# Kernel optimization log

Measured on AMD Instinct MI355X. Metric: run time of the kernel, lower is better.

## Reference

```python
import jax, jax.numpy as jnp
import numpy as np

EPS = 1e-6


def _ring_view(t, start, length, M):
    # contiguous logical view of `length` oldest positions starting at start
    if start + length <= M:
        return t[:, start:start + length]
    first = t[:, start:]
    return jnp.concatenate([first, t[:, :length - first.shape[1]]], axis=1)


def _ring_write(t, start, chunk, M):
    # write chunk at logical position `start`, wrapping around the ring
    C = chunk.shape[1]
    if start + C <= M:
        return t.at[:, start:start + C].set(chunk)
    first = M - start
    t = t.at[:, start:].set(chunk[:, :first])
    return t.at[:, :C - first].set(chunk[:, first:])


def setup_inputs() -> dict:
    key = jax.random.key(0)
    ks = jax.random.split(key, 9)
    B, M, Hh, D, F, C = 4, 1088, 32, 128, 128, 512
    f = lambda k, s: jax.random.normal(k, s, dtype=jnp.float32)
    return {
        "K": f(ks[0], (B, M, Hh, D)),
        "V": f(ks[1], (B, M, Hh, D)),
        "FK": f(ks[2], (B, M, Hh, F)),
        "H": f(ks[3], (B, Hh, F, D)),
        "S": f(ks[4], (B, Hh, F)),
        "k_c": f(ks[5], (B, C, Hh, D)),
        "v_c": f(ks[6], (B, C, Hh, D)),
        "fk_c": f(ks[7], (B, C, Hh, F)),
        "fq": f(ks[8], (B, C, Hh, F)),
        "write_ptr": 100,
        "valid": 1088,
    }


def reference(K, V, FK, H, S, k_c, v_c, fk_c, fq, write_ptr, valid):
    M = K.shape[1]
    C = k_c.shape[1]
    if valid + C <= M:
        # room left in ring buffer: plain write, no eviction
        pos = (write_ptr + valid) % M
        K = _ring_write(K, pos, k_c, M)
        V = _ring_write(V, pos, v_c, M)
        FK = _ring_write(FK, pos, fk_c, M)
    else:
        # evict num_excess oldest tokens into recurrent state H, S
        num_excess = valid + C - M
        old_fk = _ring_view(FK, write_ptr, num_excess, M)  # (B, E, H, F)
        old_v = _ring_view(V, write_ptr, num_excess, M)    # (B, E, H, D)
        H = H + jnp.einsum('behf,behd->bhfd', old_fk, old_v)
        S = S + old_fk.sum(axis=1)
        write_ptr = (write_ptr + num_excess) % M
        pos = (write_ptr + M) % M  # valid == M now
        K = _ring_write(K, pos, k_c, M)
        V = _ring_write(V, pos, v_c, M)
        FK = _ring_write(FK, pos, fk_c, M)
    # linear_attn_forward(fq)
    y_num = jnp.einsum('bchf,bhfd->bchd', fq, H)
    y_den = jnp.einsum('bchf,bhf->bch', fq, S)[..., None]
    return y_num, y_den, K, V, FK, H, S
```

## Files before the change

### kernel.cpp

```cpp
#include <hip/hip_runtime.h>

typedef float f32x4 __attribute__((ext_vector_type(4)));

constexpr int B  = 4;
constexpr int M  = 1088;
constexpr int HH = 32;
constexpr int D  = 128;
constexpr int F  = 128;
constexpr int C  = 512;

constexpr int SZ_YNUM = B * C * HH * D;
constexpr int SZ_YDEN = B * C * HH;
constexpr int SZ_KVM  = B * M * HH * D;
constexpr int SZ_H    = B * HH * F * D;
constexpr int SZ_S    = B * HH * F;

constexpr int OFF_YNUM = 0;
constexpr int OFF_YDEN = OFF_YNUM + SZ_YNUM;
constexpr int OFF_K    = OFF_YDEN + SZ_YDEN;
constexpr int OFF_V    = OFF_K + SZ_KVM;
constexpr int OFF_FK   = OFF_V + SZ_KVM;
constexpr int OFF_H    = OFF_FK + SZ_KVM;
constexpr int OFF_S    = OFF_H + SZ_H;

constexpr int INNER4      = HH * D / 4;
constexpr int ROWS_PER_CB = 4;
constexpr int COPY_BLOCKS = B * M / ROWS_PER_CB;
constexpr int EPARTS      = 4;
constexpr int HS_BLOCKS   = B * HH * 2 * EPARTS;
constexpr int Y_BLOCKS    = B * HH * 8;

__device__ __forceinline__ void ring_params(const int* wp_p, const int* valid_p,
                                            int& wp, int& num_excess, int& pos) {
    wp = *wp_p;
    int valid = *valid_p;
    if (valid + C <= M) {
        num_excess = 0;
        pos = (wp + valid) % M;
    } else {
        num_excess = valid + C - M;
        pos = (wp + num_excess) % M;
    }
}

__device__ __forceinline__ void ring_copy_block(int cb, int tid,
                                                const f32x4* __restrict__ src,
                                                const f32x4* __restrict__ chk,
                                                f32x4* __restrict__ dst,
                                                int pos) {
    int bm0 = cb * ROWS_PER_CB;
#pragma unroll
    for (int r = 0; r < ROWS_PER_CB; ++r) {
        int bm = bm0 + r;
        int m = bm % M;
        int b = bm / M;
        int off = m - pos;
        if (off < 0) off += M;
        const f32x4* s = (off < C) ? &chk[(b * C + off) * INNER4]
                                   : &src[bm * INNER4];
        f32x4* d = &dst[bm * INNER4];
#pragma unroll
        for (int k = 0; k < INNER4 / 256; ++k)
            d[k * 256 + tid] = s[k * 256 + tid];
    }
}

constexpr int ESTEP = 16;

__device__ void hs_partial_body(int bx,
                                const float* __restrict__ FKi,
                                const float* __restrict__ Vi,
                                float* __restrict__ wsH,
                                float* __restrict__ wsS,
                                int wp, int num_excess) {
    const int tid = threadIdx.x;
    const int epart = bx & (EPARTS - 1);
    int rest = bx >> 2;
    const int fhalf = rest & 1;
    const int bh = rest >> 1;
    const int h = bh & (HH - 1);
    const int b = bh >> 5;
    const int fbase = fhalf * 64;

    const int echunk = (num_excess + EPARTS * ESTEP - 1) / (EPARTS * ESTEP) * ESTEP;
    const int e_lo = epart * echunk;
    const int e_hi_raw = e_lo + echunk;
    const int e_hi = (e_hi_raw < num_excess) ? e_hi_raw : num_excess;

    __shared__ float  fk_s[ESTEP][64];
    __shared__ f32x4  v_s[ESTEP][32];
    __shared__ float  sred[4][64];

    const int tf = tid >> 5;
    const int td = tid & 31;
    const int cq = tid & 63;
    const int qq = tid >> 6;

    f32x4 acc[8];
#pragma unroll
    for (int i = 0; i < 8; ++i) acc[i] = (f32x4)0.f;
    float s_part = 0.f;

    float fk_r[4];
    f32x4 v_r[2];

    auto load_tile = [&](int e0) {
#pragma unroll
        for (int j = 0; j < 4; ++j) {
            int e = e0 + qq + 4 * j;
            int me = wp + e;
            if (me >= M) me -= M;
            if (me >= M) me -= M;
            float v = 0.f;
            if (e < e_hi) v = FKi[((b * M + me) * HH + h) * F + fbase + cq];
            fk_r[j] = v;
        }
#pragma unroll
        for (int j = 0; j < 2; ++j) {
            int e = e0 + tf + 8 * j;
            int me = wp + e;
            if (me >= M) me -= M;
            if (me >= M) me -= M;
            f32x4 v = (f32x4)0.f;
            if (e < e_hi) v = *(const f32x4*)&Vi[((b * M + me) * HH + h) * D + td * 4];
            v_r[j] = v;
        }
    };
    auto store_tile = [&]() {
#pragma unroll
        for (int j = 0; j < 4; ++j) fk_s[qq + 4 * j][cq] = fk_r[j];
#pragma unroll
        for (int j = 0; j < 2; ++j) v_s[tf + 8 * j][td] = v_r[j];
    };

    if (e_lo < e_hi) {
        load_tile(e_lo);
        store_tile();
        for (int e0 = e_lo; e0 < e_hi; e0 += ESTEP) {
            bool more = (e0 + ESTEP < e_hi);
            if (more) load_tile(e0 + ESTEP);
            __syncthreads();
#pragma unroll
            for (int ee = 0; ee < ESTEP; ++ee) {
                f32x4 fa = *(const f32x4*)&fk_s[ee][tf * 8];
                f32x4 fb = *(const f32x4*)&fk_s[ee][tf * 8 + 4];
                f32x4 vv = v_s[ee][td];
                acc[0] += fa.x * vv; acc[1] += fa.y * vv;
                acc[2] += fa.z * vv; acc[3] += fa.w * vv;
                acc[4] += fb.x * vv; acc[5] += fb.y * vv;
                acc[6] += fb.z * vv; acc[7] += fb.w * vv;
            }
#pragma unroll
            for (int j = 0; j < 4; ++j) s_part += fk_s[qq * 4 + j][cq];
            __syncthreads();
            if (more) store_tile();
        }
    }

    sred[qq][cq] = s_part;
    __syncthreads();
    if (tid < 64) {
        wsS[epart * SZ_S + (b * HH + h) * F + fbase + tid] =
            sred[0][tid] + sred[1][tid] + sred[2][tid] + sred[3][tid];
    }

    float* wsHp = wsH + epart * SZ_H;
#pragma unroll
    for (int i = 0; i < 8; ++i) {
        int f = fbase + tf * 8 + i;
        int base = ((b * HH + h) * F + f) * D + td * 4;
        *(f32x4*)&wsHp[base] = acc[i];
    }
}

__device__ void compute_y_den_body(int bx,
                                   const float* __restrict__ fq,
                                   const float* __restrict__ Hi,
                                   const float* __restrict__ Si,
                                   const float* __restrict__ wsH,
                                   const float* __restrict__ wsS,
                                   float* __restrict__ Ho,
                                   float* __restrict__ So,
                                   float* __restrict__ ynum,
                                   float* __restrict__ yden) {
    const int tid = threadIdx.x;
    int t0 = bx;
    const int ct = t0 & 7; t0 >>= 3;
    const int h = t0 & (HH - 1);
    const int b = t0 >> 5;
    const int c0 = ct * 64;
    const int bh = b * HH + h;

    __shared__ float  fq_s[32][65];
    __shared__ f32x4  h_s[32][32];
    __shared__ float  S_s[128];
    __shared__ float  den_s[64][4];

    const int tc = tid >> 5;
    const int td = tid & 31;
    const int cq = tid & 63;
    const int qq = tid >> 6;

    if (tid < 128) {
        float s = Si[bh * F + tid]
                + wsS[0 * SZ_S + bh * F + tid] + wsS[1 * SZ_S + bh * F + tid]
                + wsS[2 * SZ_S + bh * F + tid] + wsS[3 * SZ_S + bh * F + tid];
        S_s[tid] = s;
        if (ct == 0) So[bh * F + tid] = s;
    }

    f32x4 acc[8];
#pragma unroll
    for (int i = 0; i < 8; ++i) acc[i] = (f32x4)0.f;
    float den_part = 0.f;

    for (int f0 = 0; f0 < F; f0 += 32) {
#pragma unroll
        for (int r = 0; r < 8; ++r) {
            int idx = tid + r * 256;
            int cc = idx >> 5, ee = idx & 31;
            fq_s[ee][cc] = fq[((b * C + c0 + cc) * HH + h) * F + f0 + ee];
        }
#pragma unroll
        for (int r = 0; r < 4; ++r) {
            int idx = tid + r * 256;
            int row = idx >> 5, col = idx & 31;
            int base = ((bh) * F + f0 + row) * D + col * 4;
            f32x4 v = *(const f32x4*)&Hi[base];
            v += *(const f32x4*)&wsH[0 * SZ_H + base];
            v += *(const f32x4*)&wsH[1 * SZ_H + base];
            v += *(const f32x4*)&wsH[2 * SZ_H + base];
            v += *(const f32x4*)&wsH[3 * SZ_H + base];
            h_s[row][col] = v;
            if (ct == 0) *(f32x4*)&Ho[base] = v;
        }
        __syncthreads();
#pragma unroll
        for (int ee = 0; ee < 32; ++ee) {
            f32x4 hv = h_s[ee][td];
#pragma unroll
            for (int i = 0; i < 8; ++i) {
                float q = fq_s[ee][tc * 8 + i];
                acc[i] += q * hv;
            }
        }
#pragma unroll
        for (int j = 0; j < 8; ++j)
            den_part += fq_s[qq * 8 + j][cq] * S_s[f0 + qq * 8 + j];
        __syncthreads();
    }

    den_s[cq][qq] = den_part;
    __syncthreads();
    if (tid < 64)
        yden[(b * C + c0 + tid) * HH + h] =
            den_s[tid][0] + den_s[tid][1] + den_s[tid][2] + den_s[tid][3];

#pragma unroll
    for (int i = 0; i < 8; ++i) {
        int c = c0 + tc * 8 + i;
        int base = ((b * C + c) * HH + h) * D + td * 4;
        *(f32x4*)&ynum[base] = acc[i];
    }
}

__global__ __launch_bounds__(256) void fused_hs_vfk(
        const float* __restrict__ FKi, const float* __restrict__ Vi,
        float* __restrict__ wsH,       float* __restrict__ wsS,
        const f32x4* __restrict__ V4,  const f32x4* __restrict__ vc,  f32x4* __restrict__ oV,
        const f32x4* __restrict__ FK4, const f32x4* __restrict__ fkc, f32x4* __restrict__ oFK,
        const int* __restrict__ wp_p,  const int* __restrict__ valid_p) {
    int wp, num_excess, pos;
    ring_params(wp_p, valid_p, wp, num_excess, pos);

    int bx = blockIdx.x;
    if (bx < HS_BLOCKS) {
        hs_partial_body(bx, FKi, Vi, wsH, wsS, wp, num_excess);
        return;
    }
    bx -= HS_BLOCKS;
    if (bx < COPY_BLOCKS) {
        ring_copy_block(bx, threadIdx.x, V4, vc, oV, pos);
        return;
    }
    bx -= COPY_BLOCKS;
    ring_copy_block(bx, threadIdx.x, FK4, fkc, oFK, pos);
}

__global__ __launch_bounds__(256) void fused_y_k(
        const float* __restrict__ fq, const float* __restrict__ Hi,
        const float* __restrict__ Si,
        const float* __restrict__ wsH, const float* __restrict__ wsS,
        float* __restrict__ Ho,        float* __restrict__ So,
        float* __restrict__ ynum,      float* __restrict__ yden,
        const f32x4* __restrict__ K4,  const f32x4* __restrict__ kc,
        f32x4* __restrict__ oK,
        const int* __restrict__ wp_p,  const int* __restrict__ valid_p) {
    int wp, num_excess, pos;
    ring_params(wp_p, valid_p, wp, num_excess, pos);

    int bx = blockIdx.x;
    if (bx < Y_BLOCKS) {
        compute_y_den_body(bx, fq, Hi, Si, wsH, wsS, Ho, So, ynum, yden);
        return;
    }
    bx -= Y_BLOCKS;
    ring_copy_block(bx, threadIdx.x, K4, kc, oK, pos);
}

extern "C" void kernel_launch(void* const* d_in, const int* in_sizes, int n_in,
                              void* d_out, int out_size, void* d_ws, size_t ws_size,
                              hipStream_t stream) {
    const float* K   = (const float*)d_in[0];
    const float* V   = (const float*)d_in[1];
    const float* FK  = (const float*)d_in[2];
    const float* H   = (const float*)d_in[3];
    const float* S   = (const float*)d_in[4];
    const float* k_c = (const float*)d_in[5];
    const float* v_c = (const float*)d_in[6];
    const float* fk_c= (const float*)d_in[7];
    const float* fq  = (const float*)d_in[8];
    const int* wp    = (const int*)d_in[9];
    const int* valid = (const int*)d_in[10];

    float* out = (float*)d_out;
    float* o_ynum = out + OFF_YNUM;
    float* o_yden = out + OFF_YDEN;
    float* o_K    = out + OFF_K;
    float* o_V    = out + OFF_V;
    float* o_FK   = out + OFF_FK;
    float* o_H    = out + OFF_H;
    float* o_S    = out + OFF_S;

    float* wsH = (float*)d_ws;
    float* wsS = wsH + EPARTS * SZ_H;

    fused_hs_vfk<<<HS_BLOCKS + 2 * COPY_BLOCKS, 256, 0, stream>>>(
        FK, V, wsH, wsS,
        (const f32x4*)V,  (const f32x4*)v_c,  (f32x4*)o_V,
        (const f32x4*)FK, (const f32x4*)fk_c, (f32x4*)o_FK,
        wp, valid);

    fused_y_k<<<Y_BLOCKS + COPY_BLOCKS, 256, 0, stream>>>(
        fq, H, S, wsH, wsS, o_H, o_S, o_ynum, o_yden,
        (const f32x4*)K, (const f32x4*)k_c, (f32x4*)o_K,
        wp, valid);
}
```

Before: 157.5 us.

## Split H/S reduction into its own pass and double-buffer the H accumulation tiles

```diff
diff --git a/kernel.cpp b/kernel.cpp
--- a/kernel.cpp
+++ b/kernel.cpp
@@ -29,6 +29,7 @@
 constexpr int EPARTS      = 4;
 constexpr int HS_BLOCKS   = B * HH * 2 * EPARTS;
 constexpr int Y_BLOCKS    = B * HH * 8;
+constexpr int RED_BLOCKS  = 256;
 
 __device__ __forceinline__ void ring_params(const int* wp_p, const int* valid_p,
                                             int& wp, int& num_excess, int& pos) {
@@ -87,8 +88,8 @@
     const int e_hi_raw = e_lo + echunk;
     const int e_hi = (e_hi_raw < num_excess) ? e_hi_raw : num_excess;
 
-    __shared__ float  fk_s[ESTEP][64];
-    __shared__ f32x4  v_s[ESTEP][32];
+    __shared__ float  fk_s[2][ESTEP][64];
+    __shared__ f32x4  v_s[2][ESTEP][32];
     __shared__ float  sred[4][64];
 
     const int tf = tid >> 5;
@@ -101,10 +102,10 @@
     for (int i = 0; i < 8; ++i) acc[i] = (f32x4)0.f;
     float s_part = 0.f;
 
-    float fk_r[4];
-    f32x4 v_r[2];
-
-    auto load_tile = [&](int e0) {
+    float fkA[4], fkB[4];
+    f32x4 vA[2],  vB[2];
+
+    auto load_tile = [&](int e0, float* fk_r, f32x4* v_r) {
 #pragma unroll
         for (int j = 0; j < 4; ++j) {
             int e = e0 + qq + 4 * j;
@@ -126,34 +127,42 @@
             v_r[j] = v;
         }
     };
-    auto store_tile = [&]() {
-#pragma unroll
-        for (int j = 0; j < 4; ++j) fk_s[qq + 4 * j][cq] = fk_r[j];
-#pragma unroll
-        for (int j = 0; j < 2; ++j) v_s[tf + 8 * j][td] = v_r[j];
+    auto store_tile = [&](const float* fk_r, const f32x4* v_r, int buf) {
+#pragma unroll
+        for (int j = 0; j < 4; ++j) fk_s[buf][qq + 4 * j][cq] = fk_r[j];
+#pragma unroll
+        for (int j = 0; j < 2; ++j) v_s[buf][tf + 8 * j][td] = v_r[j];
     };
+    auto compute = [&](int buf) {
+#pragma unroll
+        for (int ee = 0; ee < ESTEP; ++ee) {
+            f32x4 fa = *(const f32x4*)&fk_s[buf][ee][tf * 8];
+            f32x4 fb = *(const f32x4*)&fk_s[buf][ee][tf * 8 + 4];
+            f32x4 vv = v_s[buf][ee][td];
+            acc[0] += fa.x * vv; acc[1] += fa.y * vv;
+            acc[2] += fa.z * vv; acc[3] += fa.w * vv;
+            acc[4] += fb.x * vv; acc[5] += fb.y * vv;
+            acc[6] += fb.z * vv; acc[7] += fb.w * vv;
+        }
+#pragma unroll
+        for (int j = 0; j < 4; ++j) s_part += fk_s[buf][qq * 4 + j][cq];
+    };
 
     if (e_lo < e_hi) {
-        load_tile(e_lo);
-        store_tile();
-        for (int e0 = e_lo; e0 < e_hi; e0 += ESTEP) {
-            bool more = (e0 + ESTEP < e_hi);
-            if (more) load_tile(e0 + ESTEP);
+        const int nt = (e_hi - e_lo + ESTEP - 1) / ESTEP;
+        load_tile(e_lo, fkA, vA);
+        if (nt > 1) load_tile(e_lo + ESTEP, fkB, vB);
+        store_tile(fkA, vA, 0);
+        for (int t = 0; t < nt; t += 2) {
             __syncthreads();
-#pragma unroll
-            for (int ee = 0; ee < ESTEP; ++ee) {
-                f32x4 fa = *(const f32x4*)&fk_s[ee][tf * 8];
-                f32x4 fb = *(const f32x4*)&fk_s[ee][tf * 8 + 4];
-                f32x4 vv = v_s[ee][td];
-                acc[0] += fa.x * vv; acc[1] += fa.y * vv;
-                acc[2] += fa.z * vv; acc[3] += fa.w * vv;
-                acc[4] += fb.x * vv; acc[5] += fb.y * vv;
-                acc[6] += fb.z * vv; acc[7] += fb.w * vv;
-            }
-#pragma unroll
-            for (int j = 0; j < 4; ++j) s_part += fk_s[qq * 4 + j][cq];
+            if (t + 1 < nt) store_tile(fkB, vB, 1);
+            if (t + 2 < nt) load_tile(e_lo + (t + 2) * ESTEP, fkA, vA);
+            compute(0);
+            if (t + 1 >= nt) break;
             __syncthreads();
-            if (more) store_tile();
+            if (t + 2 < nt) store_tile(fkA, vA, 0);
+            if (t + 3 < nt) load_tile(e_lo + (t + 3) * ESTEP, fkB, vB);
+            compute(1);
         }
     }
 
@@ -175,12 +184,8 @@
 
 __device__ void compute_y_den_body(int bx,
                                    const float* __restrict__ fq,
-                                   const float* __restrict__ Hi,
-                                   const float* __restrict__ Si,
-                                   const float* __restrict__ wsH,
-                                   const float* __restrict__ wsS,
-                                   float* __restrict__ Ho,
-                                   float* __restrict__ So,
+                                   const float* __restrict__ Hn,
+                                   const float* __restrict__ Sn,
                                    float* __restrict__ ynum,
                                    float* __restrict__ yden) {
     const int tid = threadIdx.x;
@@ -201,13 +206,7 @@
     const int cq = tid & 63;
     const int qq = tid >> 6;
 
-    if (tid < 128) {
-        float s = Si[bh * F + tid]
-                + wsS[0 * SZ_S + bh * F + tid] + wsS[1 * SZ_S + bh * F + tid]
-                + wsS[2 * SZ_S + bh * F + tid] + wsS[3 * SZ_S + bh * F + tid];
-        S_s[tid] = s;
-        if (ct == 0) So[bh * F + tid] = s;
-    }
+    if (tid < 128) S_s[tid] = Sn[bh * F + tid];
 
     f32x4 acc[8];
 #pragma unroll
@@ -225,14 +224,7 @@
         for (int r = 0; r < 4; ++r) {
             int idx = tid + r * 256;
             int row = idx >> 5, col = idx & 31;
-            int base = ((bh) * F + f0 + row) * D + col * 4;
-            f32x4 v = *(const f32x4*)&Hi[base];
-            v += *(const f32x4*)&wsH[0 * SZ_H + base];
-            v += *(const f32x4*)&wsH[1 * SZ_H + base];
-            v += *(const f32x4*)&wsH[2 * SZ_H + base];
-            v += *(const f32x4*)&wsH[3 * SZ_H + base];
-            h_s[row][col] = v;
-            if (ct == 0) *(f32x4*)&Ho[base] = v;
+            h_s[row][col] = *(const f32x4*)&Hn[(bh * F + f0 + row) * D + col * 4];
         }
         __syncthreads();
 #pragma unroll
@@ -287,12 +279,10 @@
     ring_copy_block(bx, threadIdx.x, FK4, fkc, oFK, pos);
 }
 
-__global__ __launch_bounds__(256) void fused_y_k(
-        const float* __restrict__ fq, const float* __restrict__ Hi,
-        const float* __restrict__ Si,
+__global__ __launch_bounds__(256) void fused_red_k(
+        const float* __restrict__ Hi,  const float* __restrict__ Si,
         const float* __restrict__ wsH, const float* __restrict__ wsS,
         float* __restrict__ Ho,        float* __restrict__ So,
-        float* __restrict__ ynum,      float* __restrict__ yden,
         const f32x4* __restrict__ K4,  const f32x4* __restrict__ kc,
         f32x4* __restrict__ oK,
         const int* __restrict__ wp_p,  const int* __restrict__ valid_p) {
@@ -300,12 +290,39 @@
     ring_params(wp_p, valid_p, wp, num_excess, pos);
 
     int bx = blockIdx.x;
-    if (bx < Y_BLOCKS) {
-        compute_y_den_body(bx, fq, Hi, Si, wsH, wsS, Ho, So, ynum, yden);
+    const int tid = threadIdx.x;
+    if (bx < RED_BLOCKS) {
+        constexpr int H4 = SZ_H / 4;
+        const f32x4* h4 = (const f32x4*)Hi;
+        const f32x4* w4 = (const f32x4*)wsH;
+        f32x4* o4 = (f32x4*)Ho;
+        int base = bx * (H4 / RED_BLOCKS) + tid;
+#pragma unroll
+        for (int r = 0; r < H4 / RED_BLOCKS / 256; ++r) {
+            int i = base + r * 256;
+            f32x4 v = h4[i];
+            v += w4[0 * H4 + i];
+            v += w4[1 * H4 + i];
+            v += w4[2 * H4 + i];
+            v += w4[3 * H4 + i];
+            o4[i] = v;
+        }
+        if (bx < SZ_S / 256) {
+            int si = bx * 256 + tid;
+            So[si] = Si[si] + wsS[si] + wsS[SZ_S + si]
+                   + wsS[2 * SZ_S + si] + wsS[3 * SZ_S + si];
+        }
         return;
     }
-    bx -= Y_BLOCKS;
-    ring_copy_block(bx, threadIdx.x, K4, kc, oK, pos);
+    bx -= RED_BLOCKS;
+    ring_copy_block(bx, tid, K4, kc, oK, pos);
+}
+
+__global__ __launch_bounds__(256) void y_kernel(
+        const float* __restrict__ fq, const float* __restrict__ Hn,
+        const float* __restrict__ Sn,
+        float* __restrict__ ynum,     float* __restrict__ yden) {
+    compute_y_den_body(blockIdx.x, fq, Hn, Sn, ynum, yden);
 }
 
 extern "C" void kernel_launch(void* const* d_in, const int* in_sizes, int n_in,
@@ -341,8 +358,10 @@
         (const f32x4*)FK, (const f32x4*)fk_c, (f32x4*)o_FK,
         wp, valid);
 
-    fused_y_k<<<Y_BLOCKS + COPY_BLOCKS, 256, 0, stream>>>(
-        fq, H, S, wsH, wsS, o_H, o_S, o_ynum, o_yden,
+    fused_red_k<<<RED_BLOCKS + COPY_BLOCKS, 256, 0, stream>>>(
+        H, S, wsH, wsS, o_H, o_S,
         (const f32x4*)K, (const f32x4*)k_c, (f32x4*)o_K,
         wp, valid);
-}
+
+    y_kernel<<<Y_BLOCKS, 256, 0, stream>>>(fq, o_H, o_S, o_ynum, o_yden);
+}
```

Measured after the change: 163.6 us, median of 4. +3.9%, slower.

## Reduce H/S partials in a separate kernel and halve eviction partitions

Applied to the files above, without the earlier changes.

```diff
diff --git a/kernel.cpp b/kernel.cpp
--- a/kernel.cpp
+++ b/kernel.cpp
@@ -26,9 +26,10 @@
 constexpr int INNER4      = HH * D / 4;
 constexpr int ROWS_PER_CB = 4;
 constexpr int COPY_BLOCKS = B * M / ROWS_PER_CB;
-constexpr int EPARTS      = 4;
+constexpr int EPARTS      = 2;
 constexpr int HS_BLOCKS   = B * HH * 2 * EPARTS;
 constexpr int Y_BLOCKS    = B * HH * 8;
+constexpr int RED_BLOCKS  = 256;
 
 __device__ __forceinline__ void ring_params(const int* wp_p, const int* valid_p,
                                             int& wp, int& num_excess, int& pos) {
@@ -75,7 +76,7 @@
                                 int wp, int num_excess) {
     const int tid = threadIdx.x;
     const int epart = bx & (EPARTS - 1);
-    int rest = bx >> 2;
+    int rest = bx >> 1;
     const int fhalf = rest & 1;
     const int bh = rest >> 1;
     const int h = bh & (HH - 1);
@@ -175,12 +176,8 @@
 
 __device__ void compute_y_den_body(int bx,
                                    const float* __restrict__ fq,
-                                   const float* __restrict__ Hi,
-                                   const float* __restrict__ Si,
-                                   const float* __restrict__ wsH,
-                                   const float* __restrict__ wsS,
-                                   float* __restrict__ Ho,
-                                   float* __restrict__ So,
+                                   const float* __restrict__ Hn,
+                                   const float* __restrict__ Sn,
                                    float* __restrict__ ynum,
                                    float* __restrict__ yden) {
     const int tid = threadIdx.x;
@@ -201,13 +198,7 @@
     const int cq = tid & 63;
     const int qq = tid >> 6;
 
-    if (tid < 128) {
-        float s = Si[bh * F + tid]
-                + wsS[0 * SZ_S + bh * F + tid] + wsS[1 * SZ_S + bh * F + tid]
-                + wsS[2 * SZ_S + bh * F + tid] + wsS[3 * SZ_S + bh * F + tid];
-        S_s[tid] = s;
-        if (ct == 0) So[bh * F + tid] = s;
-    }
+    if (tid < 128) S_s[tid] = Sn[bh * F + tid];
 
     f32x4 acc[8];
 #pragma unroll
@@ -225,14 +216,7 @@
         for (int r = 0; r < 4; ++r) {
             int idx = tid + r * 256;
             int row = idx >> 5, col = idx & 31;
-            int base = ((bh) * F + f0 + row) * D + col * 4;
-            f32x4 v = *(const f32x4*)&Hi[base];
-            v += *(const f32x4*)&wsH[0 * SZ_H + base];
-            v += *(const f32x4*)&wsH[1 * SZ_H + base];
-            v += *(const f32x4*)&wsH[2 * SZ_H + base];
-            v += *(const f32x4*)&wsH[3 * SZ_H + base];
-            h_s[row][col] = v;
-            if (ct == 0) *(f32x4*)&Ho[base] = v;
+            h_s[row][col] = *(const f32x4*)&Hn[(bh * F + f0 + row) * D + col * 4];
         }
         __syncthreads();
 #pragma unroll
@@ -287,21 +271,42 @@
     ring_copy_block(bx, threadIdx.x, FK4, fkc, oFK, pos);
 }
 
+__global__ __launch_bounds__(256) void red_kernel(
+        const float* __restrict__ Hi,  const float* __restrict__ Si,
+        const float* __restrict__ wsH, const float* __restrict__ wsS,
+        float* __restrict__ Ho,        float* __restrict__ So) {
+    const int bx = blockIdx.x;
+    const int tid = threadIdx.x;
+    constexpr int H4 = SZ_H / 4;
+    const f32x4* h4 = (const f32x4*)Hi;
+    const f32x4* w4 = (const f32x4*)wsH;
+    f32x4* o4 = (f32x4*)Ho;
+    int base = bx * (H4 / RED_BLOCKS) + tid;
+#pragma unroll
+    for (int r = 0; r < H4 / RED_BLOCKS / 256; ++r) {
+        int i = base + r * 256;
+        f32x4 v = h4[i] + w4[i] + w4[H4 + i];
+        o4[i] = v;
+    }
+    if (bx < SZ_S / 256) {
+        int si = bx * 256 + tid;
+        So[si] = Si[si] + wsS[si] + wsS[SZ_S + si];
+    }
+}
+
 __global__ __launch_bounds__(256) void fused_y_k(
-        const float* __restrict__ fq, const float* __restrict__ Hi,
-        const float* __restrict__ Si,
-        const float* __restrict__ wsH, const float* __restrict__ wsS,
-        float* __restrict__ Ho,        float* __restrict__ So,
-        float* __restrict__ ynum,      float* __restrict__ yden,
-        const f32x4* __restrict__ K4,  const f32x4* __restrict__ kc,
+        const float* __restrict__ fq, const float* __restrict__ Hn,
+        const float* __restrict__ Sn,
+        float* __restrict__ ynum,     float* __restrict__ yden,
+        const f32x4* __restrict__ K4, const f32x4* __restrict__ kc,
         f32x4* __restrict__ oK,
-        const int* __restrict__ wp_p,  const int* __restrict__ valid_p) {
+        const int* __restrict__ wp_p, const int* __restrict__ valid_p) {
     int wp, num_excess, pos;
     ring_params(wp_p, valid_p, wp, num_excess, pos);
 
     int bx = blockIdx.x;
     if (bx < Y_BLOCKS) {
-        compute_y_den_body(bx, fq, Hi, Si, wsH, wsS, Ho, So, ynum, yden);
+        compute_y_den_body(bx, fq, Hn, Sn, ynum, yden);
         return;
     }
     bx -= Y_BLOCKS;
@@ -341,8 +346,10 @@
         (const f32x4*)FK, (const f32x4*)fk_c, (f32x4*)o_FK,
         wp, valid);
 
+    red_kernel<<<RED_BLOCKS, 256, 0, stream>>>(H, S, wsH, wsS, o_H, o_S);
+
     fused_y_k<<<Y_BLOCKS + COPY_BLOCKS, 256, 0, stream>>>(
-        fq, H, S, wsH, wsS, o_H, o_S, o_ynum, o_yden,
+        fq, o_H, o_S, o_ynum, o_yden,
         (const f32x4*)K, (const f32x4*)k_c, (f32x4*)o_K,
         wp, valid);
 }
```

After: 147.0 us. 6.7% less time.
